# Kernel tuning notes

Measured on AMD Instinct MI355X. Metric: run time of the kernel, lower is better.

## Reference

```python
import jax, jax.numpy as jnp
import numpy as np

D = 2048      # hidden dim
H = 16        # heads
BSZ = 4       # batch
L = 2048      # seq len
BASE_DT = 0.1


def setup_inputs() -> dict:
    key = jax.random.key(0)
    ks = jax.random.split(key, 9)
    s = 1.0 / np.sqrt(D)
    x = jax.random.normal(ks[0], (BSZ, L, D), dtype=jnp.float32)
    v = jax.random.normal(ks[1], (BSZ, L, D), dtype=jnp.float32)
    force = jax.random.normal(ks[2], (BSZ, L, D), dtype=jnp.float32)
    WA = jax.random.normal(ks[3], (D, D), dtype=jnp.float32) * s
    bA = jnp.zeros((D,), dtype=jnp.float32)
    WB = jax.random.normal(ks[4], (D, D), dtype=jnp.float32) * s
    bB = jnp.zeros((D,), dtype=jnp.float32)
    Wdt = jax.random.normal(ks[5], (D, D), dtype=jnp.float32) * s
    bdt = jnp.zeros((D,), dtype=jnp.float32)
    # base_dt_scales buffer: 1.5**head_index, repeated head_dim times
    scales = jnp.repeat(1.5 ** jnp.arange(H, dtype=jnp.float32), D // H)
    return {"x": x, "v": v, "force": force, "WA": WA, "bA": bA,
            "WB": WB, "bB": bB, "Wdt": Wdt, "bdt": bdt, "scales": scales}


def _combine(e1, e2):
    # associative op for v_t = a_t * v_{t-1} + b_t ; e1 is the earlier element
    a1, b1 = e1
    a2, b2 = e2
    return a1 * a2, a2 * b1 + b2


def reference(x, v, force, WA, bA, WB, bB, Wdt, bdt, scales):
    # x is LayerNorm-ed in the original but the result is unused; v is unused.
    A = jax.nn.sigmoid(force @ WA + bA)                      # [B, L, D] in (0,1)
    dt = jax.nn.softplus(force @ Wdt + bdt) * BASE_DT * scales  # per-head dt scaling
    B_val = (force @ WB + bB) * dt
    # parallel associative scan over the sequence axis: v_t = A_t v_{t-1} + B_t
    _, v_seq = jax.lax.associative_scan(_combine, (A, B_val), axis=1)
    # second scan has A=1 -> plain prefix sum
    x_seq = jnp.cumsum(v_seq * dt, axis=1)
    return x_seq, v_seq
```

## Files before the change

kernel.cpp:

```cpp
#include <hip/hip_runtime.h>
#include <hip/hip_bf16.h>
#include <cstdint>
#include <cstddef>

#define D_DIM 2048
#define L_SEQ 2048
#define B_SZ 4
#define M_ROWS (B_SZ * L_SEQ)
#define NT_COLS (3 * D_DIM)
#define NCH 16
#define CHUNK (L_SEQ / NCH)

typedef __bf16 bf16_t;
typedef bf16_t bf16x8 __attribute__((ext_vector_type(8)));
typedef float f32x4 __attribute__((ext_vector_type(4)));

__device__ __forceinline__ void gl_lds16(const void* g, void* l) {
    __builtin_amdgcn_global_load_lds(
        (const __attribute__((address_space(1))) unsigned int*)g,
        (__attribute__((address_space(3))) unsigned int*)l, 16, 0, 0);
}

#define BAR()    asm volatile("s_barrier" ::: "memory")
#define VMCNT0() asm volatile("s_waitcnt vmcnt(0)" ::: "memory")

__global__ __launch_bounds__(256) void cvt_bf16_kernel(
    const float* __restrict__ in, bf16_t* __restrict__ out, int n8)
{
    int i = blockIdx.x * 256 + threadIdx.x;
    if (i >= n8) return;
    float4 f0 = ((const float4*)in)[2 * i];
    float4 f1 = ((const float4*)in)[2 * i + 1];
    bf16x8 o;
    o[0] = (bf16_t)f0.x; o[1] = (bf16_t)f0.y; o[2] = (bf16_t)f0.z; o[3] = (bf16_t)f0.w;
    o[4] = (bf16_t)f1.x; o[5] = (bf16_t)f1.y; o[6] = (bf16_t)f1.z; o[7] = (bf16_t)f1.w;
    ((bf16x8*)out)[i] = o;
}

__global__ __launch_bounds__(256) void transpose_w_kernel(
    const float* __restrict__ W0, const float* __restrict__ W1,
    const float* __restrict__ W2, bf16_t* __restrict__ Wt)
{
    __shared__ float tile[32][33];
    const float* W = (blockIdx.z == 0) ? W0 : (blockIdx.z == 1) ? W1 : W2;
    bf16_t* dst = Wt + (size_t)blockIdx.z * D_DIM * D_DIM;
    int j0 = blockIdx.x * 32, k0 = blockIdx.y * 32;
    int tx = threadIdx.x, ty = threadIdx.y;
#pragma unroll
    for (int i = 0; i < 4; i++) {
        int k = k0 + ty + i * 8;
        tile[ty + i * 8][tx] = W[(size_t)k * D_DIM + j0 + tx];
    }
    __syncthreads();
#pragma unroll
    for (int i = 0; i < 4; i++) {
        int j = j0 + ty + i * 8;
        dst[(size_t)j * D_DIM + k0 + tx] = (bf16_t)tile[tx][ty + i * 8];
    }
}

#define STAGE(LA, LB, T) {                                                     \
    const size_t kofs_ = (size_t)(T) * 64;                                     \
    _Pragma("unroll") for (int j = 0; j < 4; j++) {                            \
        gl_lds16(Abf + (size_t)(bm0 + j * 32 + srow) * D_DIM + kofs_ + scol,   \
                 (LA) + j * 2048 + w * 512);                                   \
        gl_lds16(Wt  + (size_t)(bn0 + j * 32 + srow) * D_DIM + kofs_ + scol,   \
                 (LB) + j * 2048 + w * 512);                                   \
    } }

#define COMPUTE(LA, LB) {                                                      \
    bf16x8 af[4], bfr[4];                                                      \
    _Pragma("unroll") for (int m = 0; m < 4; m++)                              \
        af[m] = *(const bf16x8*)&(LA)[(wr + m * 16) * 64 + lof0];              \
    _Pragma("unroll") for (int n = 0; n < 4; n++)                              \
        bfr[n] = *(const bf16x8*)&(LB)[(wc + n * 16) * 64 + lof0];             \
    __builtin_amdgcn_s_setprio(1);                                             \
    _Pragma("unroll") for (int m = 0; m < 4; m++)                              \
        _Pragma("unroll") for (int n = 0; n < 4; n++)                          \
            acc[m][n] = __builtin_amdgcn_mfma_f32_16x16x32_bf16(               \
                af[m], bfr[n], acc[m][n], 0, 0, 0);                            \
    __builtin_amdgcn_s_setprio(0);                                             \
    _Pragma("unroll") for (int m = 0; m < 4; m++)                              \
        af[m] = *(const bf16x8*)&(LA)[(wr + m * 16) * 64 + lof1];              \
    _Pragma("unroll") for (int n = 0; n < 4; n++)                              \
        bfr[n] = *(const bf16x8*)&(LB)[(wc + n * 16) * 64 + lof1];             \
    __builtin_amdgcn_s_setprio(1);                                             \
    _Pragma("unroll") for (int m = 0; m < 4; m++)                              \
        _Pragma("unroll") for (int n = 0; n < 4; n++)                          \
            acc[m][n] = __builtin_amdgcn_mfma_f32_16x16x32_bf16(               \
                af[m], bfr[n], acc[m][n], 0, 0, 0);                            \
    __builtin_amdgcn_s_setprio(0);                                             \
}

__global__ __launch_bounds__(256) void gemm_fused_kernel(
    const bf16_t* __restrict__ Abf,
    const bf16_t* __restrict__ Wt,
    const float* __restrict__ bA, const float* __restrict__ bdt,
    const float* __restrict__ bB, const float* __restrict__ scales,
    float* __restrict__ outA,
    float* __restrict__ outDT,
    float* __restrict__ outB)
{
    __shared__ bf16_t lds_a[2][128 * 64];
    __shared__ bf16_t lds_b[2][128 * 64];

    const int bm0 = blockIdx.x * 128;
    const int bn0 = blockIdx.y * 128;
    const int t = threadIdx.x;
    const int lane = t & 63, w = t >> 6;
    const int wr = (w >> 1) * 64;
    const int wc = (w & 1) * 64;

    f32x4 acc[4][4] = {};

    const int srow = t >> 3;
    const int scol = (((t & 7) ^ ((t >> 3) & 7)) << 3);
    const int frow = lane & 15;
    const int q = lane >> 4;
    const int fx7 = frow & 7;
    const int lof0 = frow * 64 + (((q) ^ fx7) << 3);
    const int lof1 = frow * 64 + (((4 + q) ^ fx7) << 3);

    STAGE(lds_a[0], lds_b[0], 0);
    VMCNT0();
    BAR();

#pragma unroll 1
    for (int i = 0; i < 16; ++i) {
        const int tt = 2 * i;
        STAGE(lds_a[1], lds_b[1], tt + 1);
        COMPUTE(lds_a[0], lds_b[0]);
        VMCNT0();
        BAR();
        if (i < 15) STAGE(lds_a[0], lds_b[0], tt + 2);
        COMPUTE(lds_a[1], lds_b[1]);
        VMCNT0();
        BAR();
    }

    const int seg = bn0 >> 11;
    const int dbase = (bn0 & 2047) + wc + (lane & 15);
    const int rowbase = bm0 + wr + ((lane >> 4) << 2);

    if (seg == 0) {
        float bias[4];
#pragma unroll
        for (int n = 0; n < 4; n++) bias[n] = bA[dbase + n * 16];
#pragma unroll
        for (int m = 0; m < 4; m++)
#pragma unroll
            for (int n = 0; n < 4; n++)
#pragma unroll
                for (int r = 0; r < 4; r++) {
                    size_t idx = (size_t)(rowbase + m * 16 + r) * D_DIM + dbase + n * 16;
                    outA[idx] = 1.0f / (1.0f + __expf(-(acc[m][n][r] + bias[n])));
                }
    } else if (seg == 1) {
        float bias[4], sc[4];
#pragma unroll
        for (int n = 0; n < 4; n++) { bias[n] = bdt[dbase + n * 16]; sc[n] = scales[dbase + n * 16]; }
#pragma unroll
        for (int m = 0; m < 4; m++)
#pragma unroll
            for (int n = 0; n < 4; n++)
#pragma unroll
                for (int r = 0; r < 4; r++) {
                    size_t idx = (size_t)(rowbase + m * 16 + r) * D_DIM + dbase + n * 16;
                    float xx = acc[m][n][r] + bias[n];
                    float sp = xx > 0.f ? xx + log1pf(__expf(-xx)) : log1pf(__expf(xx));
                    outDT[idx] = sp * 0.1f * sc[n];
                }
    } else {
        float bias[4];
#pragma unroll
        for (int n = 0; n < 4; n++) bias[n] = bB[dbase + n * 16];
#pragma unroll
        for (int m = 0; m < 4; m++)
#pragma unroll
            for (int n = 0; n < 4; n++)
#pragma unroll
                for (int r = 0; r < 4; r++) {
                    size_t idx = (size_t)(rowbase + m * 16 + r) * D_DIM + dbase + n * 16;
                    outB[idx] = acc[m][n][r] + bias[n];
                }
    }
}

__global__ __launch_bounds__(256) void scan_pass1_kernel(
    const float* __restrict__ Aarr, const float* __restrict__ Braw,
    const float* __restrict__ dtv, float4* __restrict__ agg)
{
    int pp = blockIdx.x * 256 + threadIdx.x;
    int dp = (pp & 1023) << 1;
    int c = (pp >> 10) & (NCH - 1);
    int b = pp >> 14;
    size_t base = ((size_t)(b * L_SEQ + c * CHUNK)) * D_DIM + dp;
    float P0 = 1.f, R0 = 0.f, U0 = 0.f, W0 = 0.f;
    float P1 = 1.f, R1 = 0.f, U1 = 0.f, W1 = 0.f;
#pragma unroll 4
    for (int tt = 0; tt < CHUNK; tt++) {
        size_t idx = base + (size_t)tt * D_DIM;
        float2 a2  = *(const float2*)&Aarr[idx];
        float2 rb2 = *(const float2*)&Braw[idx];
        float2 dt2 = *(const float2*)&dtv[idx];
        float bv0 = rb2.x * dt2.x, bv1 = rb2.y * dt2.y;
        float da0 = dt2.x * a2.x,  da1 = dt2.y * a2.y;
        R0 = da0 * P0 + R0;  W0 = da0 * U0 + dt2.x * bv0 + W0;
        U0 = a2.x * U0 + bv0;  P0 = a2.x * P0;
        R1 = da1 * P1 + R1;  W1 = da1 * U1 + dt2.y * bv1 + W1;
        U1 = a2.y * U1 + bv1;  P1 = a2.y * P1;
    }
    int ch = ((b * NCH + c) << 11) + dp;
    agg[ch]     = make_float4(P0, R0, U0, W0);
    agg[ch + 1] = make_float4(P1, R1, U1, W1);
}

__global__ __launch_bounds__(256) void scan_pass2_kernel(
    const float4* __restrict__ agg, float2* __restrict__ pre)
{
    int tid = blockIdx.x * 256 + threadIdx.x;
    int d = tid & (D_DIM - 1);
    int b = tid >> 11;
    float v = 0.f, x = 0.f;
#pragma unroll
    for (int c = 0; c < NCH; c++) {
        int i = ((b * NCH + c) << 11) + d;
        float4 g = agg[i];
        pre[i] = make_float2(v, x);
        float vn = g.x * v + g.z;
        x = g.y * v + x + g.w;
        v = vn;
    }
}

__global__ __launch_bounds__(256) void scan_pass3_kernel(
    const float* __restrict__ dtv, const float2* __restrict__ pre,
    float* __restrict__ xout, float* __restrict__ vout)
{
    int pp = blockIdx.x * 256 + threadIdx.x;
    int dp = (pp & 1023) << 1;
    int c = (pp >> 10) & (NCH - 1);
    int b = pp >> 14;
    int ch = ((b * NCH + c) << 11) + dp;
    float4 pv = *(const float4*)&pre[ch];
    float v0 = pv.x, x0 = pv.y, v1 = pv.z, x1 = pv.w;
    size_t base = ((size_t)(b * L_SEQ + c * CHUNK)) * D_DIM + dp;
#pragma unroll 4
    for (int tt = 0; tt < CHUNK; tt++) {
        size_t idx = base + (size_t)tt * D_DIM;
        float2 a2  = *(const float2*)&xout[idx];
        float2 rb2 = *(const float2*)&vout[idx];
        float2 dt2 = *(const float2*)&dtv[idx];
        v0 = a2.x * v0 + rb2.x * dt2.x;
        x0 = x0 + v0 * dt2.x;
        v1 = a2.y * v1 + rb2.y * dt2.y;
        x1 = x1 + v1 * dt2.y;
        *(float2*)&vout[idx] = make_float2(v0, v1);
        *(float2*)&xout[idx] = make_float2(x0, x1);
    }
}

extern "C" void kernel_launch(void* const* d_in, const int* in_sizes, int n_in,
                              void* d_out, int out_size, void* d_ws, size_t ws_size,
                              hipStream_t stream) {
    const float* force  = (const float*)d_in[2];
    const float* WA     = (const float*)d_in[3];
    const float* bA     = (const float*)d_in[4];
    const float* WB     = (const float*)d_in[5];
    const float* bB     = (const float*)d_in[6];
    const float* Wdt    = (const float*)d_in[7];
    const float* bdt    = (const float*)d_in[8];
    const float* scales = (const float*)d_in[9];

    float* xout = (float*)d_out;
    float* vout = xout + (size_t)M_ROWS * D_DIM;

    char* ws = (char*)d_ws;
    bf16_t* fbf = (bf16_t*)ws;
    bf16_t* wt  = (bf16_t*)(ws + (size_t)33554432);
    float*  dtv = (float*)(ws + (size_t)33554432 + 25165824);
    float4* agg = (float4*)(ws + (size_t)33554432 + 25165824 + 67108864);
    float2* pre = (float2*)(ws + (size_t)33554432 + 25165824 + 67108864 + 2097152);

    {
        int n8 = M_ROWS * D_DIM / 8;
        cvt_bf16_kernel<<<n8 / 256, 256, 0, stream>>>(force, fbf, n8);
    }
    {
        dim3 grid(D_DIM / 32, D_DIM / 32, 3), block(32, 8);
        transpose_w_kernel<<<grid, block, 0, stream>>>(WA, Wdt, WB, wt);
    }
    {
        dim3 grid(M_ROWS / 128, NT_COLS / 128);
        gemm_fused_kernel<<<grid, 256, 0, stream>>>(fbf, wt, bA, bdt, bB, scales,
                                                    xout, dtv, vout);
    }
    scan_pass1_kernel<<<(B_SZ * NCH * D_DIM / 2) / 256, 256, 0, stream>>>(xout, vout, dtv, agg);
    scan_pass2_kernel<<<(B_SZ * D_DIM) / 256, 256, 0, stream>>>(agg, pre);
    scan_pass3_kernel<<<(B_SZ * NCH * D_DIM / 2) / 256, 256, 0, stream>>>(dtv, pre, xout, vout);
}
```

Baseline: 426.4 us.

## Load A fragments directly into registers, keep only B tiles in LDS

The A operand fragments now go straight from global memory into registers, double-buffered across k-steps, and only the B weight tiles are staged through LDS. This halves LDS use and removes the LDS reads for A, which may allow higher occupancy and less LDS bandwidth pressure. The main loop is peeled so the last iteration carries no conditional, and B global addresses are precomputed per thread. In exchange, A reads become per-lane global loads, with possible duplication across the two waves that share rows, and more registers are held.

```diff
diff --git a/kernel.cpp b/kernel.cpp
--- a/kernel.cpp
+++ b/kernel.cpp
@@ -59,36 +59,36 @@
     }
 }
 
-#define STAGE(LA, LB, T) {                                                     \
+#define STAGE_B(LB, T) {                                                       \
     const size_t kofs_ = (size_t)(T) * 64;                                     \
-    _Pragma("unroll") for (int j = 0; j < 4; j++) {                            \
-        gl_lds16(Abf + (size_t)(bm0 + j * 32 + srow) * D_DIM + kofs_ + scol,   \
-                 (LA) + j * 2048 + w * 512);                                   \
-        gl_lds16(Wt  + (size_t)(bn0 + j * 32 + srow) * D_DIM + kofs_ + scol,   \
-                 (LB) + j * 2048 + w * 512);                                   \
+    _Pragma("unroll") for (int j = 0; j < 4; j++)                              \
+        gl_lds16(gB[j] + kofs_, (LB) + j * 2048 + w * 512);                    \
+}
+
+#define LOAD_A(AR, T) {                                                        \
+    const size_t kofs_ = (size_t)(T) * 64;                                     \
+    _Pragma("unroll") for (int m = 0; m < 4; m++) {                            \
+        AR##_##0[m] = *(const bf16x8*)(gA[m] + kofs_);                         \
+        AR##_##1[m] = *(const bf16x8*)(gA[m] + kofs_ + 32);                    \
     } }
 
-#define COMPUTE(LA, LB) {                                                      \
-    bf16x8 af[4], bfr[4];                                                      \
-    _Pragma("unroll") for (int m = 0; m < 4; m++)                              \
-        af[m] = *(const bf16x8*)&(LA)[(wr + m * 16) * 64 + lof0];              \
+#define COMPUTE_B(LB, AR) {                                                    \
+    bf16x8 bfr[4];                                                             \
     _Pragma("unroll") for (int n = 0; n < 4; n++)                              \
         bfr[n] = *(const bf16x8*)&(LB)[(wc + n * 16) * 64 + lof0];             \
     __builtin_amdgcn_s_setprio(1);                                             \
     _Pragma("unroll") for (int m = 0; m < 4; m++)                              \
         _Pragma("unroll") for (int n = 0; n < 4; n++)                          \
             acc[m][n] = __builtin_amdgcn_mfma_f32_16x16x32_bf16(               \
-                af[m], bfr[n], acc[m][n], 0, 0, 0);                            \
+                AR##_##0[m], bfr[n], acc[m][n], 0, 0, 0);                      \
     __builtin_amdgcn_s_setprio(0);                                             \
-    _Pragma("unroll") for (int m = 0; m < 4; m++)                              \
-        af[m] = *(const bf16x8*)&(LA)[(wr + m * 16) * 64 + lof1];              \
     _Pragma("unroll") for (int n = 0; n < 4; n++)                              \
         bfr[n] = *(const bf16x8*)&(LB)[(wc + n * 16) * 64 + lof1];             \
     __builtin_amdgcn_s_setprio(1);                                             \
     _Pragma("unroll") for (int m = 0; m < 4; m++)                              \
         _Pragma("unroll") for (int n = 0; n < 4; n++)                          \
             acc[m][n] = __builtin_amdgcn_mfma_f32_16x16x32_bf16(               \
-                af[m], bfr[n], acc[m][n], 0, 0, 0);                            \
+                AR##_##1[m], bfr[n], acc[m][n], 0, 0, 0);                      \
     __builtin_amdgcn_s_setprio(0);                                             \
 }
 
@@ -101,8 +101,8 @@
     float* __restrict__ outDT,
     float* __restrict__ outB)
 {
-    __shared__ bf16_t lds_a[2][128 * 64];
-    __shared__ bf16_t lds_b[2][128 * 64];
+    __shared__ bf16_t lds_b0[128 * 64];
+    __shared__ bf16_t lds_b1[128 * 64];
 
     const int bm0 = blockIdx.x * 128;
     const int bn0 = blockIdx.y * 128;
@@ -115,32 +115,53 @@
 
     const int srow = t >> 3;
     const int scol = (((t & 7) ^ ((t >> 3) & 7)) << 3);
+    const bf16_t* gB[4];
+#pragma unroll
+    for (int j = 0; j < 4; j++)
+        gB[j] = Wt + (size_t)(bn0 + j * 32 + srow) * D_DIM + scol;
+
     const int frow = lane & 15;
     const int q = lane >> 4;
     const int fx7 = frow & 7;
     const int lof0 = frow * 64 + (((q) ^ fx7) << 3);
     const int lof1 = frow * 64 + (((4 + q) ^ fx7) << 3);
 
-    STAGE(lds_a[0], lds_b[0], 0);
+    const bf16_t* gA[4];
+#pragma unroll
+    for (int m = 0; m < 4; m++)
+        gA[m] = Abf + (size_t)(bm0 + wr + m * 16 + frow) * D_DIM + q * 8;
+
+    bf16x8 a0_0[4], a0_1[4], a1_0[4], a1_1[4];
+
+    STAGE_B(lds_b0, 0);
+    LOAD_A(a0, 0);
     VMCNT0();
     BAR();
 
 #pragma unroll 1
-    for (int i = 0; i < 16; ++i) {
+    for (int i = 0; i < 15; ++i) {
         const int tt = 2 * i;
-        STAGE(lds_a[1], lds_b[1], tt + 1);
-        COMPUTE(lds_a[0], lds_b[0]);
+        STAGE_B(lds_b1, tt + 1);
+        LOAD_A(a1, tt + 1);
+        COMPUTE_B(lds_b0, a0);
         VMCNT0();
         BAR();
-        if (i < 15) STAGE(lds_a[0], lds_b[0], tt + 2);
-        COMPUTE(lds_a[1], lds_b[1]);
+        STAGE_B(lds_b0, tt + 2);
+        LOAD_A(a0, tt + 2);
+        COMPUTE_B(lds_b1, a1);
         VMCNT0();
         BAR();
     }
+    STAGE_B(lds_b1, 31);
+    LOAD_A(a1, 31);
+    COMPUTE_B(lds_b0, a0);
+    VMCNT0();
+    BAR();
+    COMPUTE_B(lds_b1, a1);
 
     const int seg = bn0 >> 11;
     const int dbase = (bn0 & 2047) + wc + (lane & 15);
-    const int rowbase = bm0 + wr + ((lane >> 4) << 2);
+    const int rowbase = bm0 + wr + (q << 2);
 
     if (seg == 0) {
         float bias[4];
```

New measurement: 888.3 us. 2.08x slower.

## Enlarge GEMM block tile to 256x256 with 16 waves per block

Applied to the files above, without the earlier changes.

The fused GEMM block tile grows from 128x128 to 256x256 and runs 1024 threads (16 waves in a 4x4 grid), each wave still owning a 64x64 sub-tile. Global staging addresses are precomputed once per thread, and the final K iteration is peeled so the loop no longer branches. The aim is more reuse of each staged A/W tile per byte of global traffic. In exchange the block uses 128KB of LDS and the grid has a quarter as many blocks, which may reduce occupancy and latency hiding.

```diff
diff --git a/kernel.cpp b/kernel.cpp
--- a/kernel.cpp
+++ b/kernel.cpp
@@ -61,11 +61,9 @@
 
 #define STAGE(LA, LB, T) {                                                     \
     const size_t kofs_ = (size_t)(T) * 64;                                     \
-    _Pragma("unroll") for (int j = 0; j < 4; j++) {                            \
-        gl_lds16(Abf + (size_t)(bm0 + j * 32 + srow) * D_DIM + kofs_ + scol,   \
-                 (LA) + j * 2048 + w * 512);                                   \
-        gl_lds16(Wt  + (size_t)(bn0 + j * 32 + srow) * D_DIM + kofs_ + scol,   \
-                 (LB) + j * 2048 + w * 512);                                   \
+    _Pragma("unroll") for (int j = 0; j < 2; j++) {                            \
+        gl_lds16(gA[j] + kofs_, (LA) + j * 8192 + w * 512);                    \
+        gl_lds16(gB[j] + kofs_, (LB) + j * 8192 + w * 512);                    \
     } }
 
 #define COMPUTE(LA, LB) {                                                      \
@@ -92,7 +90,7 @@
     __builtin_amdgcn_s_setprio(0);                                             \
 }
 
-__global__ __launch_bounds__(256) void gemm_fused_kernel(
+__global__ __launch_bounds__(1024) void gemm_fused_kernel(
     const bf16_t* __restrict__ Abf,
     const bf16_t* __restrict__ Wt,
     const float* __restrict__ bA, const float* __restrict__ bdt,
@@ -101,46 +99,61 @@
     float* __restrict__ outDT,
     float* __restrict__ outB)
 {
-    __shared__ bf16_t lds_a[2][128 * 64];
-    __shared__ bf16_t lds_b[2][128 * 64];
-
-    const int bm0 = blockIdx.x * 128;
-    const int bn0 = blockIdx.y * 128;
+    __shared__ bf16_t lds_a0[256 * 64];
+    __shared__ bf16_t lds_a1[256 * 64];
+    __shared__ bf16_t lds_b0[256 * 64];
+    __shared__ bf16_t lds_b1[256 * 64];
+
+    const int bm0 = blockIdx.x * 256;
+    const int bn0 = blockIdx.y * 256;
     const int t = threadIdx.x;
     const int lane = t & 63, w = t >> 6;
-    const int wr = (w >> 1) * 64;
-    const int wc = (w & 1) * 64;
+    const int wr = (w >> 2) * 64;
+    const int wc = (w & 3) * 64;
 
     f32x4 acc[4][4] = {};
 
     const int srow = t >> 3;
     const int scol = (((t & 7) ^ ((t >> 3) & 7)) << 3);
+    const bf16_t* gA[2];
+    const bf16_t* gB[2];
+#pragma unroll
+    for (int j = 0; j < 2; j++) {
+        gA[j] = Abf + (size_t)(bm0 + j * 128 + srow) * D_DIM + scol;
+        gB[j] = Wt + (size_t)(bn0 + j * 128 + srow) * D_DIM + scol;
+    }
+
     const int frow = lane & 15;
     const int q = lane >> 4;
     const int fx7 = frow & 7;
     const int lof0 = frow * 64 + (((q) ^ fx7) << 3);
     const int lof1 = frow * 64 + (((4 + q) ^ fx7) << 3);
 
-    STAGE(lds_a[0], lds_b[0], 0);
+    STAGE(lds_a0, lds_b0, 0);
     VMCNT0();
     BAR();
 
 #pragma unroll 1
-    for (int i = 0; i < 16; ++i) {
+    for (int i = 0; i < 15; ++i) {
         const int tt = 2 * i;
-        STAGE(lds_a[1], lds_b[1], tt + 1);
-        COMPUTE(lds_a[0], lds_b[0]);
+        STAGE(lds_a1, lds_b1, tt + 1);
+        COMPUTE(lds_a0, lds_b0);
         VMCNT0();
         BAR();
-        if (i < 15) STAGE(lds_a[0], lds_b[0], tt + 2);
-        COMPUTE(lds_a[1], lds_b[1]);
+        STAGE(lds_a0, lds_b0, tt + 2);
+        COMPUTE(lds_a1, lds_b1);
         VMCNT0();
         BAR();
     }
+    STAGE(lds_a1, lds_b1, 31);
+    COMPUTE(lds_a0, lds_b0);
+    VMCNT0();
+    BAR();
+    COMPUTE(lds_a1, lds_b1);
 
     const int seg = bn0 >> 11;
     const int dbase = (bn0 & 2047) + wc + (lane & 15);
-    const int rowbase = bm0 + wr + ((lane >> 4) << 2);
+    const int rowbase = bm0 + wr + (q << 2);
 
     if (seg == 0) {
         float bias[4];
@@ -291,9 +304,9 @@
         transpose_w_kernel<<<grid, block, 0, stream>>>(WA, Wdt, WB, wt);
     }
     {
-        dim3 grid(M_ROWS / 128, NT_COLS / 128);
-        gemm_fused_kernel<<<grid, 256, 0, stream>>>(fbf, wt, bA, bdt, bB, scales,
-                                                    xout, dtv, vout);
+        dim3 grid(M_ROWS / 256, NT_COLS / 256);
+        gemm_fused_kernel<<<grid, 1024, 0, stream>>>(fbf, wt, bA, bdt, bB, scales,
+                                                     xout, dtv, vout);
     }
     scan_pass1_kernel<<<(B_SZ * NCH * D_DIM / 2) / 256, 256, 0, stream>>>(xout, vout, dtv, agg);
     scan_pass2_kernel<<<(B_SZ * D_DIM) / 256, 256, 0, stream>>>(agg, pre);
```

After: 419.9 us. No clear change (-1.5%).
